# Performance work log

Hardware: AMD Instinct MI355X
Metric: run time of the kernel (lower is better)

## Reference

```python
import math
import jax, jax.numpy as jnp
import numpy as np

B, S, D = 2, 2048, 1024
H, DK = 16, 64
NUM_BUCKETS = 32
MAX_DISTANCE = 128


def _relative_position_bucket(relative_position, num_buckets=NUM_BUCKETS, max_distance=MAX_DISTANCE):
    # bidirectional=True branch (encoder / non-causal)
    n = -relative_position
    num_buckets = num_buckets // 2
    ret = (n < 0).astype(jnp.int32) * num_buckets
    n = jnp.abs(n)
    max_exact = num_buckets // 2
    is_small = n < max_exact
    # guard log(0); masked out by is_small anyway
    n_safe = jnp.maximum(n, 1).astype(jnp.float32)
    val_if_large = max_exact + (
        jnp.log(n_safe / max_exact) / math.log(max_distance / max_exact) * (num_buckets - max_exact)
    ).astype(jnp.int32)
    val_if_large = jnp.minimum(val_if_large, num_buckets - 1)
    return ret + jnp.where(is_small, n, val_if_large)


def setup_inputs() -> dict:
    key = jax.random.key(0)
    ks = jax.random.split(key, 6)
    std_q = (D * DK) ** -0.5
    std = D ** -0.5
    return {
        "x": jax.random.normal(ks[0], (B, S, D), jnp.float32),
        "q_w": jax.random.normal(ks[1], (H * DK, D), jnp.float32) * std_q,
        "k_w": jax.random.normal(ks[2], (H * DK, D), jnp.float32) * std,
        "v_w": jax.random.normal(ks[3], (H * DK, D), jnp.float32) * std,
        "o_w": jax.random.normal(ks[4], (D, H * DK), jnp.float32) * ((H * DK) ** -0.5),
        "rel_bias": jax.random.normal(ks[5], (NUM_BUCKETS, H), jnp.float32) * std,
    }


def reference(x, q_w, k_w, v_w, o_w, rel_bias):
    b, s, _ = x.shape
    # project and split heads: [B, H, S, DK]
    def proj(w):
        return (x @ w.T).reshape(b, s, H, DK).transpose(0, 2, 1, 3)
    q, k, v = proj(q_w), proj(k_w), proj(v_w)

    # T5-style unscaled attention scores: [B, H, Sq, Sk]
    scores = jnp.einsum("bhqd,bhkd->bhqk", q, k)

    # bucketed relative-position bias
    ctx = jnp.arange(s)[:, None]
    mem = jnp.arange(s)[None, :]
    rp_bucket = _relative_position_bucket(mem - ctx)  # [S, S]
    bias = rel_bias[rp_bucket]                        # [S, S, H]
    bias = bias.transpose(2, 0, 1)[None]              # [1, H, S, S]
    scores = scores + bias

    attn = jax.nn.softmax(scores, axis=-1)
    ctx_out = jnp.einsum("bhqk,bhkd->bhqd", attn, v)
    ctx_out = ctx_out.transpose(0, 2, 1, 3).reshape(b, s, H * DK)
    return ctx_out @ o_w.T
```

## Files before the change

kernel.cpp:

```cpp
#include <hip/hip_runtime.h>
#include <stdint.h>


typedef unsigned short u16;
typedef __attribute__((ext_vector_type(8))) short short8;
typedef __attribute__((ext_vector_type(4))) float float4v;
typedef __attribute__((ext_vector_type(4))) u16 ushort4v;
typedef __attribute__((ext_vector_type(4))) uint32_t uint4v;

typedef __attribute__((address_space(1))) void void_g;
typedef __attribute__((address_space(3))) void void_l;

#define L2E 1.4426950408889634f

__device__ __forceinline__ u16 f2b(float f) {
  union { float f; uint32_t u; } v; v.f = f;
  uint32_t r = (v.u + 0x7fffu + ((v.u >> 16) & 1u)) >> 16;
  return (u16)r;
}
__device__ __forceinline__ u16 f2b_fast(float f) {
  union { float f; uint32_t u; } v; v.f = f;
  return (u16)((v.u + 0x8000u) >> 16);
}
__device__ __forceinline__ uint32_t cvt_pk_bf16(float lo, float hi) {
  uint32_t r;
  asm("v_cvt_pk_bf16_f32 %0, %1, %2" : "=v"(r) : "v"(lo), "v"(hi));
  return r;
}

__global__ void cvt_all(const float* __restrict__ x,  const float* __restrict__ qw,
                        const float* __restrict__ kw, const float* __restrict__ vw,
                        const float* __restrict__ ow, const float* __restrict__ rel_bias,
                        u16* __restrict__ xb, u16* __restrict__ wqkv, u16* __restrict__ owb,
                        float* __restrict__ biasT) {
  int bi = blockIdx.x;
  if (bi >= 8192) {
    int idx = (bi - 8192) * 256 + threadIdx.x;
    int h = idx >> 12, t = idx & 4095;
    if (t > 4094) { biasT[h * 4096 + 4095] = -1.0e4f; return; }
    int d = t - 2047;
    int n = -d;
    int ret = (n < 0) ? 16 : 0;
    int na = (n < 0) ? -n : n;
    int bucket;
    if (na < 8) {
      bucket = ret + na;
    } else {
      float v = logf((float)na / 8.0f) / logf(16.0f) * 8.0f;
      int vi = 8 + (int)v;
      bucket = ret + (vi > 15 ? 15 : vi);
    }
    biasT[h * 4096 + t] = (rel_bias[bucket * 16 + h] - 8.0f) * L2E;
    return;
  }
  int i = bi * 256 + threadIdx.x;
  const float* s; u16* d; int off;
  if (i < 1048576)      { s = x;  d = xb;              off = i; }
  else if (i < 1310720) { s = qw; d = wqkv;            off = i - 1048576; }
  else if (i < 1572864) { s = kw; d = wqkv + 1048576;  off = i - 1310720; }
  else if (i < 1835008) { s = vw; d = wqkv + 2097152;  off = i - 1572864; }
  else                  { s = ow; d = owb;             off = i - 1835008; }
  float4v v = ((const float4v*)s)[off];
  ushort4v o;
  o.x = f2b(v.x); o.y = f2b(v.y); o.z = f2b(v.z); o.w = f2b(v.w);
  ((ushort4v*)d)[off] = o;
}

__global__ __launch_bounds__(256, 3)
void gemm_qkv(const u16* __restrict__ A, const u16* __restrict__ W,
              u16* __restrict__ qkb, u16* __restrict__ vTp) {
  const int K = 1024;
  __shared__ __align__(16) char SM[34816];
  u16* As = (u16*)SM;
  u16* Bs = (u16*)(SM + 16384);
  const int tid = threadIdx.x;
  const int wid = tid >> 6;
  const int lane = tid & 63;
  const int row16 = lane & 15, oct = lane >> 4;
  const int lin = blockIdx.x + blockIdx.y * 32;
  const int V = (lin & 7) * 96 + (lin >> 3);
  const int bx = V & 31, by = V >> 5;
  const int tm = bx * 128, tn = by * 128;
  const int wm = (wid & 1) * 64, wn = (wid >> 1) * 64;
  const int srow = lane >> 2;
  const int sc = (lane & 3) * 8;
  float4v acc[4][4] = {};
  for (int k0 = 0; k0 < K; k0 += 64) {
    __syncthreads();
#pragma unroll
    for (int i = 0; i < 4; i++) {
      const int idx = i * 4 + wid;
      const int kk = idx & 1;
      const int rb = idx >> 1;
      const int r = rb * 16 + srow;
      const int c = kk * 32 + sc;
      __builtin_amdgcn_global_load_lds((void_g*)(A + (size_t)(tm + r) * K + k0 + c),
                                       (void_l*)(As + (kk * 128 + rb * 16) * 32), 16, 0, 0);
      __builtin_amdgcn_global_load_lds((void_g*)(W + (size_t)(tn + r) * K + k0 + c),
                                       (void_l*)(Bs + (kk * 128 + rb * 16) * 32), 16, 0, 0);
    }
    __syncthreads();
#pragma unroll
    for (int kk = 0; kk < 2; kk++) {
      short8 af[4], bfr[4];
#pragma unroll
      for (int mi = 0; mi < 4; mi++)
        af[mi] = *(const short8*)(As + (kk * 128 + wm + mi * 16 + row16) * 32 + oct * 8);
#pragma unroll
      for (int ni = 0; ni < 4; ni++)
        bfr[ni] = *(const short8*)(Bs + (kk * 128 + wn + ni * 16 + row16) * 32 + oct * 8);
#pragma unroll
      for (int mi = 0; mi < 4; mi++)
#pragma unroll
        for (int ni = 0; ni < 4; ni++)
          acc[mi][ni] = __builtin_amdgcn_mfma_f32_16x16x32_bf16(af[mi], bfr[ni], acc[mi][ni], 0, 0, 0);
    }
  }

  if (tn < 2048) {
    u16* Es = (u16*)SM;
    __syncthreads();
#pragma unroll
    for (int mi = 0; mi < 4; mi++)
#pragma unroll
      for (int ni = 0; ni < 4; ni++)
#pragma unroll
        for (int r = 0; r < 4; r++)
          Es[(wm + mi * 16 + oct * 4 + r) * 136 + wn + ni * 16 + row16] = f2b(acc[mi][ni][r]);
    __syncthreads();
#pragma unroll
    for (int it = 0; it < 8; it++) {
      int idx = it * 256 + tid;
      int row = idx >> 4, c = idx & 15;
      short8 v = *(const short8*)(Es + row * 136 + c * 8);
      *(short8*)(qkb + (size_t)(tm + row) * 2048 + tn + c * 8) = v;
    }
  } else {
    const int h0 = (tn - 2048) >> 6;
    const int b = tm >> 11;
    const int s0 = tm & 2047;
#pragma unroll
    for (int ni = 0; ni < 4; ni++) {
      const int dg = wn + ni * 16 + row16;
      const int head = h0 + (dg >> 6), d = dg & 63;
      u16* vdst = vTp + ((size_t)((b * 16 + head) * 64 + d)) * 2048 + s0 + wm + oct * 8;
#pragma unroll
      for (int bb = 0; bb < 2; bb++) {
        uint4v pw;
        pw.x = cvt_pk_bf16(acc[2 * bb][ni][0], acc[2 * bb][ni][1]);
        pw.y = cvt_pk_bf16(acc[2 * bb][ni][2], acc[2 * bb][ni][3]);
        pw.z = cvt_pk_bf16(acc[2 * bb + 1][ni][0], acc[2 * bb + 1][ni][1]);
        pw.w = cvt_pk_bf16(acc[2 * bb + 1][ni][2], acc[2 * bb + 1][ni][3]);
        *(uint4v*)(vdst + bb * 32) = pw;
      }
    }
  }
}

__global__ __launch_bounds__(256, 2)
void gemm_out(const u16* __restrict__ A, const u16* __restrict__ W,
              float* __restrict__ C) {
  const int K = 1024, N = 1024;
  __shared__ __align__(16) char SM[49152];
  const int tid = threadIdx.x;
  const int wid = tid >> 6;
  const int lane = tid & 63;
  const int row16 = lane & 15, oct = lane >> 4;
  const int tm = blockIdx.x * 64, tn = blockIdx.y * 128;
  const int wm = (wid & 1) * 32, wn = (wid >> 1) * 64;
  const int srow = lane >> 2;
  const int sc = (lane & 3) * 8;
  float4v acc[2][4] = {};

#define STAGE_OUT(buf, k0)                                                            \
  {                                                                                   \
    u16* Ad = (u16*)(SM + (buf) * 24576);                                             \
    u16* Bd = (u16*)(SM + (buf) * 24576 + 8192);                                      \
    _Pragma("unroll")                                                                 \
    for (int i = 0; i < 2; i++) {                                                     \
      const int idx = i * 4 + wid;                                                    \
      const int kk = idx & 1;                                                         \
      const int rb = idx >> 1;                                                        \
      const int r = rb * 16 + srow;                                                   \
      const int c = kk * 32 + sc;                                                     \
      __builtin_amdgcn_global_load_lds((void_g*)(A + (size_t)(tm + r) * K + (k0) + c),\
                                       (void_l*)(Ad + (kk * 64 + rb * 16) * 32), 16, 0, 0); \
    }                                                                                 \
    _Pragma("unroll")                                                                 \
    for (int i = 0; i < 4; i++) {                                                     \
      const int idx = i * 4 + wid;                                                    \
      const int kk = idx & 1;                                                         \
      const int rb = idx >> 1;                                                        \
      const int r = rb * 16 + srow;                                                   \
      const int c = kk * 32 + sc;                                                     \
      __builtin_amdgcn_global_load_lds((void_g*)(W + (size_t)(tn + r) * K + (k0) + c),\
                                       (void_l*)(Bd + (kk * 128 + rb * 16) * 32), 16, 0, 0); \
    }                                                                                 \
  }

  STAGE_OUT(0, 0);
  __syncthreads();
  for (int t = 0; t < 16; t++) {
    if (t + 1 < 16) STAGE_OUT((t + 1) & 1, (t + 1) * 64);
    const u16* As = (const u16*)(SM + (t & 1) * 24576);
    const u16* Bs = As + 4096;
#pragma unroll
    for (int kk = 0; kk < 2; kk++) {
      short8 af[2], bfr[4];
#pragma unroll
      for (int mi = 0; mi < 2; mi++)
        af[mi] = *(const short8*)(As + (kk * 64 + wm + mi * 16 + row16) * 32 + oct * 8);
#pragma unroll
      for (int ni = 0; ni < 4; ni++)
        bfr[ni] = *(const short8*)(Bs + (kk * 128 + wn + ni * 16 + row16) * 32 + oct * 8);
#pragma unroll
      for (int mi = 0; mi < 2; mi++)
#pragma unroll
        for (int ni = 0; ni < 4; ni++)
          acc[mi][ni] = __builtin_amdgcn_mfma_f32_16x16x32_bf16(af[mi], bfr[ni], acc[mi][ni], 0, 0, 0);
    }
    __syncthreads();
  }
  float* Ef = (float*)SM;
#pragma unroll
  for (int mi = 0; mi < 2; mi++)
#pragma unroll
    for (int ni = 0; ni < 4; ni++)
#pragma unroll
      for (int r = 0; r < 4; r++)
        Ef[(wm + mi * 16 + oct * 4 + r) * 132 + wn + ni * 16 + row16] = acc[mi][ni][r];
  __syncthreads();
#pragma unroll
  for (int it = 0; it < 8; it++) {
    int idx = it * 256 + tid;
    int row = idx >> 5, c = idx & 31;
    float4v v = *(const float4v*)(Ef + row * 132 + c * 4);
    *(float4v*)(C + (size_t)(tm + row) * N + tn + c * 4) = v;
  }
}

__global__ __launch_bounds__(256, 2)
void flash_attn(const u16* __restrict__ qkb, const u16* __restrict__ vTp,
                const float* __restrict__ biasT, u16* __restrict__ ctx) {
  const int S = 2048, LDQ = 2048;
  const int lin = blockIdx.x + (blockIdx.y << 4) + (blockIdx.z << 8);
  const int V = (lin & 7) * 64 + (lin >> 3);
  const int qt0 = (V & 15) * 128;
  const int h = (V >> 4) & 15, b = V >> 8;
  const int tid = threadIdx.x, wid = tid >> 6, lane = tid & 63;
  const int row16 = lane & 15, oct = lane >> 4;

  __shared__ __align__(16) float biasS[2176];
  __shared__ __align__(16) u16 Ks[2][64][40];
  __shared__ __align__(16) u16 Vts[2][64][40];

  {
    const float* bsrc = biasT + h * 4096 + (1920 - qt0);
    for (int i = tid; i < 544; i += 256)
      ((float4v*)biasS)[i] = ((const float4v*)bsrc)[i];
  }
  const float bias_neg = biasT[h * 4096];
  const float bias_pos = biasT[h * 4096 + 4094];

  const u16* qbase = qkb + ((size_t)b * S + qt0 + wid * 32) * LDQ + h * 64;
  short8 qf[2][2];
#pragma unroll
  for (int f = 0; f < 2; f++)
#pragma unroll
    for (int hd = 0; hd < 2; hd++)
      qf[f][hd] = *(const short8*)(qbase + (size_t)(f * 16 + row16) * LDQ + hd * 32 + oct * 8);

  float4v l_acc[2] = {};
  float4v o_acc[2][4] = {};
  const short8 ones = {0x3F80, 0x3F80, 0x3F80, 0x3F80, 0x3F80, 0x3F80, 0x3F80, 0x3F80};

  const int sr = lane >> 2, c8 = (lane & 3) * 8;
  const int srow = wid * 16 + sr;
  const u16* Kst = qkb + 1024 + ((size_t)b * S + srow) * LDQ + c8 + h * 64;
  const u16* Vst = vTp + ((size_t)(b * 16 + h) * 64 + srow) * 2048 + c8;

  short8 kreg[2], vreg[2];
#pragma unroll
  for (int hd = 0; hd < 2; hd++) kreg[hd] = *(const short8*)(Kst + hd * 32);
#pragma unroll
  for (int ks = 0; ks < 2; ks++) vreg[ks] = *(const short8*)(Vst + ks * 32);

  for (int kt = 0; kt < S; kt += 64) {
    __syncthreads();
#pragma unroll
    for (int hd = 0; hd < 2; hd++) *(short8*)&Ks[hd][srow][c8] = kreg[hd];
#pragma unroll
    for (int ks = 0; ks < 2; ks++) *(short8*)&Vts[ks][srow][c8] = vreg[ks];
    __syncthreads();

    if (kt + 64 < S) {
#pragma unroll
      for (int hd = 0; hd < 2; hd++)
        kreg[hd] = *(const short8*)(Kst + (size_t)(kt + 64) * LDQ + hd * 32);
#pragma unroll
      for (int ks = 0; ks < 2; ks++)
        vreg[ks] = *(const short8*)(Vst + (kt + 64) + ks * 32);
    }

    short8 kf[4][2];
#pragma unroll
    for (int st = 0; st < 4; st++)
#pragma unroll
      for (int hd = 0; hd < 2; hd++)
        kf[st][hd] = *(const short8*)&Ks[hd][st * 16 + row16][oct * 8];

    float4v sc[2][4];
    __builtin_amdgcn_s_setprio(1);
#pragma unroll
    for (int f = 0; f < 2; f++)
#pragma unroll
      for (int st = 0; st < 4; st++) {
        float4v s = {};
        s = __builtin_amdgcn_mfma_f32_16x16x32_bf16(kf[st][0], qf[f][0], s, 0, 0, 0);
        s = __builtin_amdgcn_mfma_f32_16x16x32_bf16(kf[st][1], qf[f][1], s, 0, 0, 0);
        sc[f][st] = s;
      }
    __builtin_amdgcn_s_setprio(0);

    short8 vf[2][4];
#pragma unroll
    for (int ks = 0; ks < 2; ks++)
#pragma unroll
      for (int ni = 0; ni < 4; ni++)
        vf[ks][ni] = *(const short8*)&Vts[ks][ni * 16 + row16][oct * 8];

    const int dk = kt - qt0;
    const bool far = (dk >= 256) || (dk <= -192);
    if (far) {
      const float bc = (dk > 0) ? bias_pos : bias_neg;
#pragma unroll
      for (int f = 0; f < 2; f++)
#pragma unroll
        for (int st = 0; st < 4; st++)
#pragma unroll
          for (int r = 0; r < 4; r++)
            sc[f][st][r] = __builtin_amdgcn_exp2f(__builtin_fmaf(sc[f][st][r], L2E, bc));
    } else {
#pragma unroll
      for (int f = 0; f < 2; f++) {
        const int basef = kt + oct * 4 - wid * 32 - f * 16 - row16 + 127;
#pragma unroll
        for (int st = 0; st < 4; st++)
#pragma unroll
          for (int r = 0; r < 4; r++)
            sc[f][st][r] = __builtin_amdgcn_exp2f(
                __builtin_fmaf(sc[f][st][r], L2E, biasS[basef + st * 16 + r]));
      }
    }

#pragma unroll
    for (int f = 0; f < 2; f++) {
#pragma unroll
      for (int ks = 0; ks < 2; ks++) {
        uint4v pw;
        pw.x = cvt_pk_bf16(sc[f][2 * ks][0], sc[f][2 * ks][1]);
        pw.y = cvt_pk_bf16(sc[f][2 * ks][2], sc[f][2 * ks][3]);
        pw.z = cvt_pk_bf16(sc[f][2 * ks + 1][0], sc[f][2 * ks + 1][1]);
        pw.w = cvt_pk_bf16(sc[f][2 * ks + 1][2], sc[f][2 * ks + 1][3]);
        short8 pf = __builtin_bit_cast(short8, pw);
        __builtin_amdgcn_s_setprio(1);
#pragma unroll
        for (int ni = 0; ni < 4; ni++)
          o_acc[f][ni] = __builtin_amdgcn_mfma_f32_16x16x32_bf16(pf, vf[ks][ni], o_acc[f][ni], 0, 0, 0);
        l_acc[f] = __builtin_amdgcn_mfma_f32_16x16x32_bf16(pf, ones, l_acc[f], 0, 0, 0);
        __builtin_amdgcn_s_setprio(0);
      }
    }
  }

#pragma unroll
  for (int f = 0; f < 2; f++) {
    float linv[4];
#pragma unroll
    for (int r = 0; r < 4; r++)
      linv[r] = 1.0f / l_acc[f][r];
    const size_t orow = (size_t)b * S + qt0 + wid * 32 + f * 16 + oct * 4;
#pragma unroll
    for (int ni = 0; ni < 4; ni++)
#pragma unroll
      for (int r = 0; r < 4; r++)
        ctx[(orow + r) * 1024 + h * 64 + ni * 16 + row16] = f2b_fast(o_acc[f][ni][r] * linv[r]);
  }
}

extern "C" void kernel_launch(void* const* d_in, const int* in_sizes, int n_in,
                              void* d_out, int out_size, void* d_ws, size_t ws_size,
                              hipStream_t stream) {
  const float* x        = (const float*)d_in[0];
  const float* q_w      = (const float*)d_in[1];
  const float* k_w      = (const float*)d_in[2];
  const float* v_w      = (const float*)d_in[3];
  const float* o_w      = (const float*)d_in[4];
  const float* rel_bias = (const float*)d_in[5];

  char* ws = (char*)d_ws;
  u16*   xb    = (u16*)(ws);
  u16*   wqkv  = (u16*)(ws + 8388608);
  u16*   owb   = (u16*)(ws + 14680064);
  u16*   qkb   = (u16*)(ws + 16777216);
  u16*   vTp   = (u16*)(ws + 33554432);
  u16*   ctxb  = (u16*)(ws + 41943040);
  float* biasT = (float*)(ws + 50331648);

  cvt_all<<<8448, 256, 0, stream>>>(x, q_w, k_w, v_w, o_w, rel_bias,
                                    xb, wqkv, owb, biasT);

  dim3 g1(4096 / 128, 3072 / 128);
  gemm_qkv<<<g1, 256, 0, stream>>>(xb, wqkv, qkb, vTp);

  dim3 g2(2048 / 128, 16, 2);
  flash_attn<<<g2, 256, 0, stream>>>(qkb, vTp, biasT, ctxb);

  dim3 g3(4096 / 64, 1024 / 128);
  gemm_out<<<g3, 256, 0, stream>>>(ctxb, owb, (float*)d_out);
}
```

Measured before the change: 172.0 us.

## Software-pipeline QK^T of next tile with softmax/PV of current tile

Double-buffers the K and V shared-memory tiles and restructures the attention loop so the QK^T MFMAs for the next key tile are issued while the exp/bias and PV MFMAs for the current tile run. Two score register sets alternate through a manually unrolled macro body. The aim is to overlap the exp transcendental work with matrix-core work and hide LDS latency. In exchange it roughly doubles score registers and shared memory, which could hurt occupancy under launch_bounds(256,2), and it keeps two barriers per tile.

```diff
diff --git a/kernel.cpp b/kernel.cpp
--- a/kernel.cpp
+++ b/kernel.cpp
@@ -251,8 +251,8 @@
   const int row16 = lane & 15, oct = lane >> 4;
 
   __shared__ __align__(16) float biasS[2176];
-  __shared__ __align__(16) u16 Ks[2][64][40];
-  __shared__ __align__(16) u16 Vts[2][64][40];
+  __shared__ __align__(16) u16 Ks[2][2][64][40];
+  __shared__ __align__(16) u16 Vts[2][2][64][40];
 
   {
     const float* bsrc = biasT + h * 4096 + (1920 - qt0);
@@ -280,36 +280,28 @@
   const u16* Vst = vTp + ((size_t)(b * 16 + h) * 64 + srow) * 2048 + c8;
 
   short8 kreg[2], vreg[2];
+  float4v scA[2][4], scB[2][4];
+
 #pragma unroll
   for (int hd = 0; hd < 2; hd++) kreg[hd] = *(const short8*)(Kst + hd * 32);
 #pragma unroll
   for (int ks = 0; ks < 2; ks++) vreg[ks] = *(const short8*)(Vst + ks * 32);
-
-  for (int kt = 0; kt < S; kt += 64) {
-    __syncthreads();
-#pragma unroll
-    for (int hd = 0; hd < 2; hd++) *(short8*)&Ks[hd][srow][c8] = kreg[hd];
-#pragma unroll
-    for (int ks = 0; ks < 2; ks++) *(short8*)&Vts[ks][srow][c8] = vreg[ks];
-    __syncthreads();
-
-    if (kt + 64 < S) {
+#pragma unroll
+  for (int hd = 0; hd < 2; hd++) *(short8*)&Ks[0][hd][srow][c8] = kreg[hd];
+#pragma unroll
+  for (int ks = 0; ks < 2; ks++) *(short8*)&Vts[0][ks][srow][c8] = vreg[ks];
+#pragma unroll
+  for (int hd = 0; hd < 2; hd++) kreg[hd] = *(const short8*)(Kst + (size_t)64 * LDQ + hd * 32);
+#pragma unroll
+  for (int ks = 0; ks < 2; ks++) vreg[ks] = *(const short8*)(Vst + 64 + ks * 32);
+  __syncthreads();
+  {
+    short8 kf[4][2];
+#pragma unroll
+    for (int st = 0; st < 4; st++)
 #pragma unroll
       for (int hd = 0; hd < 2; hd++)
-        kreg[hd] = *(const short8*)(Kst + (size_t)(kt + 64) * LDQ + hd * 32);
-#pragma unroll
-      for (int ks = 0; ks < 2; ks++)
-        vreg[ks] = *(const short8*)(Vst + (kt + 64) + ks * 32);
-    }
-
-    short8 kf[4][2];
-#pragma unroll
-    for (int st = 0; st < 4; st++)
-#pragma unroll
-      for (int hd = 0; hd < 2; hd++)
-        kf[st][hd] = *(const short8*)&Ks[hd][st * 16 + row16][oct * 8];
-
-    float4v sc[2][4];
+        kf[st][hd] = *(const short8*)&Ks[0][hd][st * 16 + row16][oct * 8];
     __builtin_amdgcn_s_setprio(1);
 #pragma unroll
     for (int f = 0; f < 2; f++)
@@ -318,60 +310,107 @@
         float4v s = {};
         s = __builtin_amdgcn_mfma_f32_16x16x32_bf16(kf[st][0], qf[f][0], s, 0, 0, 0);
         s = __builtin_amdgcn_mfma_f32_16x16x32_bf16(kf[st][1], qf[f][1], s, 0, 0, 0);
-        sc[f][st] = s;
+        scA[f][st] = s;
       }
     __builtin_amdgcn_s_setprio(0);
-
-    short8 vf[2][4];
-#pragma unroll
-    for (int ks = 0; ks < 2; ks++)
-#pragma unroll
-      for (int ni = 0; ni < 4; ni++)
-        vf[ks][ni] = *(const short8*)&Vts[ks][ni * 16 + row16][oct * 8];
-
-    const int dk = kt - qt0;
-    const bool far = (dk >= 256) || (dk <= -192);
-    if (far) {
-      const float bc = (dk > 0) ? bias_pos : bias_neg;
-#pragma unroll
-      for (int f = 0; f < 2; f++)
-#pragma unroll
-        for (int st = 0; st < 4; st++)
-#pragma unroll
-          for (int r = 0; r < 4; r++)
-            sc[f][st][r] = __builtin_amdgcn_exp2f(__builtin_fmaf(sc[f][st][r], L2E, bc));
-    } else {
-#pragma unroll
-      for (int f = 0; f < 2; f++) {
-        const int basef = kt + oct * 4 - wid * 32 - f * 16 - row16 + 127;
-#pragma unroll
-        for (int st = 0; st < 4; st++)
-#pragma unroll
-          for (int r = 0; r < 4; r++)
-            sc[f][st][r] = __builtin_amdgcn_exp2f(
-                __builtin_fmaf(sc[f][st][r], L2E, biasS[basef + st * 16 + r]));
-      }
-    }
-
-#pragma unroll
-    for (int f = 0; f < 2; f++) {
-#pragma unroll
-      for (int ks = 0; ks < 2; ks++) {
-        uint4v pw;
-        pw.x = cvt_pk_bf16(sc[f][2 * ks][0], sc[f][2 * ks][1]);
-        pw.y = cvt_pk_bf16(sc[f][2 * ks][2], sc[f][2 * ks][3]);
-        pw.z = cvt_pk_bf16(sc[f][2 * ks + 1][0], sc[f][2 * ks + 1][1]);
-        pw.w = cvt_pk_bf16(sc[f][2 * ks + 1][2], sc[f][2 * ks + 1][3]);
-        short8 pf = __builtin_bit_cast(short8, pw);
-        __builtin_amdgcn_s_setprio(1);
-#pragma unroll
-        for (int ni = 0; ni < 4; ni++)
-          o_acc[f][ni] = __builtin_amdgcn_mfma_f32_16x16x32_bf16(pf, vf[ks][ni], o_acc[f][ni], 0, 0, 0);
-        l_acc[f] = __builtin_amdgcn_mfma_f32_16x16x32_bf16(pf, ones, l_acc[f], 0, 0, 0);
-        __builtin_amdgcn_s_setprio(0);
-      }
-    }
-  }
+  }
+
+#define FLASH_BODY(SCA, SCB, CUR, NB, KT)                                          \
+  {                                                                                \
+    const int kt_ = (KT);                                                          \
+    const bool has_next = (kt_ + 64 < S);                                          \
+    if (has_next) {                                                                \
+      _Pragma("unroll")                                                            \
+      for (int hd = 0; hd < 2; hd++) *(short8*)&Ks[NB][hd][srow][c8] = kreg[hd];   \
+      _Pragma("unroll")                                                            \
+      for (int ks = 0; ks < 2; ks++) *(short8*)&Vts[NB][ks][srow][c8] = vreg[ks];  \
+    }                                                                              \
+    __syncthreads();                                                               \
+    short8 vf[2][4];                                                               \
+    _Pragma("unroll")                                                              \
+    for (int ks = 0; ks < 2; ks++)                                                 \
+      _Pragma("unroll")                                                            \
+      for (int ni = 0; ni < 4; ni++)                                               \
+        vf[ks][ni] = *(const short8*)&Vts[CUR][ks][ni * 16 + row16][oct * 8];      \
+    short8 kf[4][2];                                                               \
+    if (has_next) {                                                                \
+      _Pragma("unroll")                                                            \
+      for (int st = 0; st < 4; st++)                                               \
+        _Pragma("unroll")                                                          \
+        for (int hd = 0; hd < 2; hd++)                                             \
+          kf[st][hd] = *(const short8*)&Ks[NB][hd][st * 16 + row16][oct * 8];      \
+    }                                                                              \
+    if (kt_ + 128 < S) {                                                           \
+      _Pragma("unroll")                                                            \
+      for (int hd = 0; hd < 2; hd++)                                               \
+        kreg[hd] = *(const short8*)(Kst + (size_t)(kt_ + 128) * LDQ + hd * 32);    \
+      _Pragma("unroll")                                                            \
+      for (int ks = 0; ks < 2; ks++)                                               \
+        vreg[ks] = *(const short8*)(Vst + (kt_ + 128) + ks * 32);                  \
+    }                                                                              \
+    const int dk = kt_ - qt0;                                                      \
+    const bool far = (dk >= 256) || (dk <= -192);                                  \
+    if (far) {                                                                     \
+      const float bc = (dk > 0) ? bias_pos : bias_neg;                             \
+      _Pragma("unroll")                                                            \
+      for (int f = 0; f < 2; f++)                                                  \
+        _Pragma("unroll")                                                          \
+        for (int st = 0; st < 4; st++)                                             \
+          _Pragma("unroll")                                                        \
+          for (int r = 0; r < 4; r++)                                              \
+            SCA[f][st][r] = __builtin_amdgcn_exp2f(                                \
+                __builtin_fmaf(SCA[f][st][r], L2E, bc));                           \
+    } else {                                                                       \
+      _Pragma("unroll")                                                            \
+      for (int f = 0; f < 2; f++) {                                                \
+        const int basef = kt_ + oct * 4 - wid * 32 - f * 16 - row16 + 127;         \
+        _Pragma("unroll")                                                          \
+        for (int st = 0; st < 4; st++)                                             \
+          _Pragma("unroll")                                                        \
+          for (int r = 0; r < 4; r++)                                              \
+            SCA[f][st][r] = __builtin_amdgcn_exp2f(                                \
+                __builtin_fmaf(SCA[f][st][r], L2E, biasS[basef + st * 16 + r]));   \
+      }                                                                            \
+    }                                                                              \
+    if (has_next) {                                                                \
+      __builtin_amdgcn_s_setprio(1);                                               \
+      _Pragma("unroll")                                                            \
+      for (int f = 0; f < 2; f++)                                                  \
+        _Pragma("unroll")                                                          \
+        for (int st = 0; st < 4; st++) {                                           \
+          float4v s = {};                                                          \
+          s = __builtin_amdgcn_mfma_f32_16x16x32_bf16(kf[st][0], qf[f][0], s, 0, 0, 0); \
+          s = __builtin_amdgcn_mfma_f32_16x16x32_bf16(kf[st][1], qf[f][1], s, 0, 0, 0); \
+          SCB[f][st] = s;                                                          \
+        }                                                                          \
+      __builtin_amdgcn_s_setprio(0);                                               \
+    }                                                                              \
+    _Pragma("unroll")                                                              \
+    for (int f = 0; f < 2; f++) {                                                  \
+      _Pragma("unroll")                                                            \
+      for (int ks = 0; ks < 2; ks++) {                                             \
+        uint4v pw;                                                                 \
+        pw.x = cvt_pk_bf16(SCA[f][2 * ks][0], SCA[f][2 * ks][1]);                  \
+        pw.y = cvt_pk_bf16(SCA[f][2 * ks][2], SCA[f][2 * ks][3]);                  \
+        pw.z = cvt_pk_bf16(SCA[f][2 * ks + 1][0], SCA[f][2 * ks + 1][1]);          \
+        pw.w = cvt_pk_bf16(SCA[f][2 * ks + 1][2], SCA[f][2 * ks + 1][3]);          \
+        short8 pf = __builtin_bit_cast(short8, pw);                                \
+        __builtin_amdgcn_s_setprio(1);                                             \
+        _Pragma("unroll")                                                          \
+        for (int ni = 0; ni < 4; ni++)                                             \
+          o_acc[f][ni] = __builtin_amdgcn_mfma_f32_16x16x32_bf16(pf, vf[ks][ni], o_acc[f][ni], 0, 0, 0); \
+        l_acc[f] = __builtin_amdgcn_mfma_f32_16x16x32_bf16(pf, ones, l_acc[f], 0, 0, 0); \
+        __builtin_amdgcn_s_setprio(0);                                             \
+      }                                                                            \
+    }                                                                              \
+    __syncthreads();                                                               \
+  }
+
+  for (int kt = 0; kt < S; kt += 128) {
+    FLASH_BODY(scA, scB, 0, 1, kt);
+    FLASH_BODY(scB, scA, 1, 0, kt + 64);
+  }
+#undef FLASH_BODY
 
 #pragma unroll
   for (int f = 0; f < 2; f++) {
```

Result: slower. 183.6 us (+6.8%).

## Double-buffer K/V tiles in flash attention and store GEMM output directly

Applied to the files above, without the earlier changes.

The flash attention loop now keeps K and V tiles in two shared-memory buffers. The next tile is written into the alternate buffer while the current one is consumed, which cuts the two barriers per iteration down to one and prefetches global loads two tiles ahead. The GEMM epilogue also drops its shared-memory staging and barrier, writing accumulators straight to global memory. The cost is uncoalesced scalar stores in the GEMM and more shared memory in attention, which could reduce occupancy.

```diff
diff --git a/kernel.cpp b/kernel.cpp
--- a/kernel.cpp
+++ b/kernel.cpp
@@ -221,22 +221,14 @@
     }
     __syncthreads();
   }
-  float* Ef = (float*)SM;
 #pragma unroll
   for (int mi = 0; mi < 2; mi++)
 #pragma unroll
     for (int ni = 0; ni < 4; ni++)
 #pragma unroll
       for (int r = 0; r < 4; r++)
-        Ef[(wm + mi * 16 + oct * 4 + r) * 132 + wn + ni * 16 + row16] = acc[mi][ni][r];
-  __syncthreads();
-#pragma unroll
-  for (int it = 0; it < 8; it++) {
-    int idx = it * 256 + tid;
-    int row = idx >> 5, c = idx & 31;
-    float4v v = *(const float4v*)(Ef + row * 132 + c * 4);
-    *(float4v*)(C + (size_t)(tm + row) * N + tn + c * 4) = v;
-  }
+        C[(size_t)(tm + wm + mi * 16 + oct * 4 + r) * N + tn + wn + ni * 16 + row16] =
+            acc[mi][ni][r];
 }
 
 __global__ __launch_bounds__(256, 2)
@@ -251,8 +243,8 @@
   const int row16 = lane & 15, oct = lane >> 4;
 
   __shared__ __align__(16) float biasS[2176];
-  __shared__ __align__(16) u16 Ks[2][64][40];
-  __shared__ __align__(16) u16 Vts[2][64][40];
+  __shared__ __align__(16) u16 Ks[2][2][64][40];
+  __shared__ __align__(16) u16 Vts[2][2][64][40];
 
   {
     const float* bsrc = biasT + h * 4096 + (1920 - qt0);
@@ -284,22 +276,31 @@
   for (int hd = 0; hd < 2; hd++) kreg[hd] = *(const short8*)(Kst + hd * 32);
 #pragma unroll
   for (int ks = 0; ks < 2; ks++) vreg[ks] = *(const short8*)(Vst + ks * 32);
+#pragma unroll
+  for (int hd = 0; hd < 2; hd++) *(short8*)&Ks[0][hd][srow][c8] = kreg[hd];
+#pragma unroll
+  for (int ks = 0; ks < 2; ks++) *(short8*)&Vts[0][ks][srow][c8] = vreg[ks];
+#pragma unroll
+  for (int hd = 0; hd < 2; hd++) kreg[hd] = *(const short8*)(Kst + (size_t)64 * LDQ + hd * 32);
+#pragma unroll
+  for (int ks = 0; ks < 2; ks++) vreg[ks] = *(const short8*)(Vst + 64 + ks * 32);
+  __syncthreads();
 
   for (int kt = 0; kt < S; kt += 64) {
-    __syncthreads();
-#pragma unroll
-    for (int hd = 0; hd < 2; hd++) *(short8*)&Ks[hd][srow][c8] = kreg[hd];
-#pragma unroll
-    for (int ks = 0; ks < 2; ks++) *(short8*)&Vts[ks][srow][c8] = vreg[ks];
-    __syncthreads();
-
+    const int cur = (kt >> 6) & 1, nb = cur ^ 1;
     if (kt + 64 < S) {
 #pragma unroll
+      for (int hd = 0; hd < 2; hd++) *(short8*)&Ks[nb][hd][srow][c8] = kreg[hd];
+#pragma unroll
+      for (int ks = 0; ks < 2; ks++) *(short8*)&Vts[nb][ks][srow][c8] = vreg[ks];
+    }
+    if (kt + 128 < S) {
+#pragma unroll
       for (int hd = 0; hd < 2; hd++)
-        kreg[hd] = *(const short8*)(Kst + (size_t)(kt + 64) * LDQ + hd * 32);
+        kreg[hd] = *(const short8*)(Kst + (size_t)(kt + 128) * LDQ + hd * 32);
 #pragma unroll
       for (int ks = 0; ks < 2; ks++)
-        vreg[ks] = *(const short8*)(Vst + (kt + 64) + ks * 32);
+        vreg[ks] = *(const short8*)(Vst + (kt + 128) + ks * 32);
     }
 
     short8 kf[4][2];
@@ -307,7 +308,7 @@
     for (int st = 0; st < 4; st++)
 #pragma unroll
       for (int hd = 0; hd < 2; hd++)
-        kf[st][hd] = *(const short8*)&Ks[hd][st * 16 + row16][oct * 8];
+        kf[st][hd] = *(const short8*)&Ks[cur][hd][st * 16 + row16][oct * 8];
 
     float4v sc[2][4];
     __builtin_amdgcn_s_setprio(1);
@@ -327,7 +328,7 @@
     for (int ks = 0; ks < 2; ks++)
 #pragma unroll
       for (int ni = 0; ni < 4; ni++)
-        vf[ks][ni] = *(const short8*)&Vts[ks][ni * 16 + row16][oct * 8];
+        vf[ks][ni] = *(const short8*)&Vts[cur][ks][ni * 16 + row16][oct * 8];
 
     const int dk = kt - qt0;
     const bool far = (dk >= 256) || (dk <= -192);
@@ -371,6 +372,7 @@
         __builtin_amdgcn_s_setprio(0);
       }
     }
+    __syncthreads();
   }
 
 #pragma unroll
```

New measurement: 171.8 us, median of 2. Within noise of the previous version (-0.1%).

## Split flash attention key range across two wave groups and drop gemm_out LDS epilogue

Applied to the files above, without the earlier changes.

The attention kernel now launches 512 threads per block, with two groups of four waves each handling half of the key sequence for the same query tile. The groups merge their unnormalised output and row-sum accumulators through shared memory at the end. Softmax uses no running max, so the partial sums can simply be added. This doubles the waves available per query tile to hide latency, at the cost of more LDS, an extra merge step and barrier, and a tighter register budget under launch_bounds(512,4). Separately, the output GEMM writes accumulators straight to global memory instead of staging them through LDS for coalesced float4 stores.

```diff
diff --git a/kernel.cpp b/kernel.cpp
--- a/kernel.cpp
+++ b/kernel.cpp
@@ -221,25 +221,17 @@
     }
     __syncthreads();
   }
-  float* Ef = (float*)SM;
 #pragma unroll
   for (int mi = 0; mi < 2; mi++)
 #pragma unroll
     for (int ni = 0; ni < 4; ni++)
 #pragma unroll
       for (int r = 0; r < 4; r++)
-        Ef[(wm + mi * 16 + oct * 4 + r) * 132 + wn + ni * 16 + row16] = acc[mi][ni][r];
-  __syncthreads();
-#pragma unroll
-  for (int it = 0; it < 8; it++) {
-    int idx = it * 256 + tid;
-    int row = idx >> 5, c = idx & 31;
-    float4v v = *(const float4v*)(Ef + row * 132 + c * 4);
-    *(float4v*)(C + (size_t)(tm + row) * N + tn + c * 4) = v;
-  }
-}
-
-__global__ __launch_bounds__(256, 2)
+        C[(size_t)(tm + wm + mi * 16 + oct * 4 + r) * N + tn + wn + ni * 16 + row16] =
+            acc[mi][ni][r];
+}
+
+__global__ __launch_bounds__(512, 4)
 void flash_attn(const u16* __restrict__ qkb, const u16* __restrict__ vTp,
                 const float* __restrict__ biasT, u16* __restrict__ ctx) {
   const int S = 2048, LDQ = 2048;
@@ -249,20 +241,23 @@
   const int h = (V >> 4) & 15, b = V >> 8;
   const int tid = threadIdx.x, wid = tid >> 6, lane = tid & 63;
   const int row16 = lane & 15, oct = lane >> 4;
-
-  __shared__ __align__(16) float biasS[2176];
-  __shared__ __align__(16) u16 Ks[2][64][40];
-  __shared__ __align__(16) u16 Vts[2][64][40];
+  const int qw = wid & 3;
+  const int half = wid >> 2;
+
+  __shared__ __align__(16) char SM[49664];
+  float* biasS = (float*)SM;
+  u16* KsB  = (u16*)(SM + 8704);
+  u16* VtsB = (u16*)(SM + 8704 + 20480);
 
   {
     const float* bsrc = biasT + h * 4096 + (1920 - qt0);
-    for (int i = tid; i < 544; i += 256)
+    for (int i = tid; i < 544; i += 512)
       ((float4v*)biasS)[i] = ((const float4v*)bsrc)[i];
   }
   const float bias_neg = biasT[h * 4096];
   const float bias_pos = biasT[h * 4096 + 4094];
 
-  const u16* qbase = qkb + ((size_t)b * S + qt0 + wid * 32) * LDQ + h * 64;
+  const u16* qbase = qkb + ((size_t)b * S + qt0 + qw * 32) * LDQ + h * 64;
   short8 qf[2][2];
 #pragma unroll
   for (int f = 0; f < 2; f++)
@@ -275,9 +270,12 @@
   const short8 ones = {0x3F80, 0x3F80, 0x3F80, 0x3F80, 0x3F80, 0x3F80, 0x3F80, 0x3F80};
 
   const int sr = lane >> 2, c8 = (lane & 3) * 8;
-  const int srow = wid * 16 + sr;
-  const u16* Kst = qkb + 1024 + ((size_t)b * S + srow) * LDQ + c8 + h * 64;
-  const u16* Vst = vTp + ((size_t)(b * 16 + h) * 64 + srow) * 2048 + c8;
+  const int srow = qw * 16 + sr;
+  const u16* Kst = qkb + 1024 + ((size_t)b * S + half * 1024 + srow) * LDQ + c8 + h * 64;
+  const u16* Vst = vTp + ((size_t)(b * 16 + h) * 64 + srow) * 2048 + half * 1024 + c8;
+
+  u16* KsH  = KsB  + half * 2 * 64 * 40;
+  u16* VtsH = VtsB + half * 2 * 64 * 40;
 
   short8 kreg[2], vreg[2];
 #pragma unroll
@@ -285,15 +283,17 @@
 #pragma unroll
   for (int ks = 0; ks < 2; ks++) vreg[ks] = *(const short8*)(Vst + ks * 32);
 
-  for (int kt = 0; kt < S; kt += 64) {
-    __syncthreads();
-#pragma unroll
-    for (int hd = 0; hd < 2; hd++) *(short8*)&Ks[hd][srow][c8] = kreg[hd];
-#pragma unroll
-    for (int ks = 0; ks < 2; ks++) *(short8*)&Vts[ks][srow][c8] = vreg[ks];
-    __syncthreads();
-
-    if (kt + 64 < S) {
+  for (int kt = 0; kt < 1024; kt += 64) {
+    __syncthreads();
+#pragma unroll
+    for (int hd = 0; hd < 2; hd++)
+      *(short8*)(KsH + (hd * 64 + srow) * 40 + c8) = kreg[hd];
+#pragma unroll
+    for (int ks = 0; ks < 2; ks++)
+      *(short8*)(VtsH + (ks * 64 + srow) * 40 + c8) = vreg[ks];
+    __syncthreads();
+
+    if (kt + 64 < 1024) {
 #pragma unroll
       for (int hd = 0; hd < 2; hd++)
         kreg[hd] = *(const short8*)(Kst + (size_t)(kt + 64) * LDQ + hd * 32);
@@ -307,7 +307,7 @@
     for (int st = 0; st < 4; st++)
 #pragma unroll
       for (int hd = 0; hd < 2; hd++)
-        kf[st][hd] = *(const short8*)&Ks[hd][st * 16 + row16][oct * 8];
+        kf[st][hd] = *(const short8*)(KsH + (hd * 64 + st * 16 + row16) * 40 + oct * 8);
 
     float4v sc[2][4];
     __builtin_amdgcn_s_setprio(1);
@@ -327,9 +327,9 @@
     for (int ks = 0; ks < 2; ks++)
 #pragma unroll
       for (int ni = 0; ni < 4; ni++)
-        vf[ks][ni] = *(const short8*)&Vts[ks][ni * 16 + row16][oct * 8];
-
-    const int dk = kt - qt0;
+        vf[ks][ni] = *(const short8*)(VtsH + (ks * 64 + ni * 16 + row16) * 40 + oct * 8);
+
+    const int dk = half * 1024 + kt - qt0;
     const bool far = (dk >= 256) || (dk <= -192);
     if (far) {
       const float bc = (dk > 0) ? bias_pos : bias_neg;
@@ -343,7 +343,7 @@
     } else {
 #pragma unroll
       for (int f = 0; f < 2; f++) {
-        const int basef = kt + oct * 4 - wid * 32 - f * 16 - row16 + 127;
+        const int basef = half * 1024 + kt + oct * 4 - qw * 32 - f * 16 - row16 + 127;
 #pragma unroll
         for (int st = 0; st < 4; st++)
 #pragma unroll
@@ -373,18 +373,37 @@
     }
   }
 
-#pragma unroll
-  for (int f = 0; f < 2; f++) {
-    float linv[4];
-#pragma unroll
-    for (int r = 0; r < 4; r++)
-      linv[r] = 1.0f / l_acc[f][r];
-    const size_t orow = (size_t)b * S + qt0 + wid * 32 + f * 16 + oct * 4;
-#pragma unroll
-    for (int ni = 0; ni < 4; ni++)
+  __syncthreads();
+  float* MRG = (float*)SM;
+  const int slot = (qw * 64 + lane) * 40;
+  if (half == 1) {
+#pragma unroll
+    for (int f = 0; f < 2; f++) {
+#pragma unroll
+      for (int ni = 0; ni < 4; ni++)
+        *(float4v*)(MRG + slot + (f * 4 + ni) * 4) = o_acc[f][ni];
+      *(float4v*)(MRG + slot + 32 + f * 4) = l_acc[f];
+    }
+  }
+  __syncthreads();
+  if (half == 0) {
+#pragma unroll
+    for (int f = 0; f < 2; f++) {
+      float4v lp = *(const float4v*)(MRG + slot + 32 + f * 4);
+      float linv[4];
 #pragma unroll
       for (int r = 0; r < 4; r++)
-        ctx[(orow + r) * 1024 + h * 64 + ni * 16 + row16] = f2b_fast(o_acc[f][ni][r] * linv[r]);
+        linv[r] = 1.0f / (l_acc[f][r] + lp[r]);
+      const size_t orow = (size_t)b * S + qt0 + qw * 32 + f * 16 + oct * 4;
+#pragma unroll
+      for (int ni = 0; ni < 4; ni++) {
+        float4v op = *(const float4v*)(MRG + slot + (f * 4 + ni) * 4);
+#pragma unroll
+        for (int r = 0; r < 4; r++)
+          ctx[(orow + r) * 1024 + h * 64 + ni * 16 + row16] =
+              f2b_fast((o_acc[f][ni][r] + op[r]) * linv[r]);
+      }
+    }
   }
 }
 
@@ -413,8 +432,8 @@
   dim3 g1(4096 / 128, 3072 / 128);
   gemm_qkv<<<g1, 256, 0, stream>>>(xb, wqkv, qkb, vTp);
 
-  dim3 g2(2048 / 128, 16, 2);
-  flash_attn<<<g2, 256, 0, stream>>>(qkb, vTp, biasT, ctxb);
+  dim3 g2(16, 16, 2);
+  flash_attn<<<g2, 512, 0, stream>>>(qkb, vTp, biasT, ctxb);
 
   dim3 g3(4096 / 64, 1024 / 128);
   gemm_out<<<g3, 256, 0, stream>>>(ctxb, owb, (float*)d_out);
```

Result: slower. 368.4 us (+114.2%).
